# Optimization experiments

Hardware: AMD Instinct MI355X
Metric: run time of the kernel (lower is better)

Reference implementation:

```python
import jax, jax.numpy as jnp
import numpy as np

H = 256
V_IN = 32000
V_OUT = 32000
T = 2048


def setup_inputs() -> dict:
    key = jax.random.key(0)
    ks = jax.random.split(key, 16)
    s = 1.0 / np.sqrt(H)
    inp = {
        "src": jax.random.randint(ks[0], (T, 1), 0, V_IN, dtype=jnp.int64 if jax.config.jax_enable_x64 else jnp.int32),
        "trg": jax.random.randint(ks[1], (T, 1), 0, V_OUT, dtype=jnp.int64 if jax.config.jax_enable_x64 else jnp.int32),
        "enc_emb": jax.random.normal(ks[2], (V_IN, H), jnp.float32),
        "enc_W_ih": jax.random.uniform(ks[3], (3 * H, H), jnp.float32, -s, s),
        "enc_W_hh": jax.random.uniform(ks[4], (3 * H, H), jnp.float32, -s, s),
        "enc_b_ih": jax.random.uniform(ks[5], (3 * H,), jnp.float32, -s, s),
        "enc_b_hh": jax.random.uniform(ks[6], (3 * H,), jnp.float32, -s, s),
        "dec_emb": jax.random.normal(ks[7], (V_OUT, H), jnp.float32),
        "dec_W_ih": jax.random.uniform(ks[8], (3 * H, H), jnp.float32, -s, s),
        "dec_W_hh": jax.random.uniform(ks[9], (3 * H, H), jnp.float32, -s, s),
        "dec_b_ih": jax.random.uniform(ks[10], (3 * H,), jnp.float32, -s, s),
        "dec_b_hh": jax.random.uniform(ks[11], (3 * H,), jnp.float32, -s, s),
        "out_W": jax.random.uniform(ks[12], (V_OUT, H), jnp.float32, -s, s),
        "out_b": jax.random.uniform(ks[13], (V_OUT,), jnp.float32, -s, s),
    }
    return inp


def _gru_step(x, h, W_ih, W_hh, b_ih, b_hh):
    # PyTorch GRU cell math. x,h: [H]
    gi = W_ih @ x + b_ih          # [3H]
    gh = W_hh @ h + b_hh          # [3H]
    i_r, i_z, i_n = jnp.split(gi, 3)
    h_r, h_z, h_n = jnp.split(gh, 3)
    r = jax.nn.sigmoid(i_r + h_r)
    z = jax.nn.sigmoid(i_z + h_z)
    n = jnp.tanh(i_n + r * h_n)
    return (1.0 - z) * n + z * h


def reference(src, trg, enc_emb, enc_W_ih, enc_W_hh, enc_b_ih, enc_b_hh,
              dec_emb, dec_W_ih, dec_W_hh, dec_b_ih, dec_b_hh, out_W, out_b):
    src_t = src[:, 0]  # [T], batch forced to 1 by .view(1,1,-1)
    trg_t = trg[:, 0]  # [T]
    h0 = jnp.zeros((H,), enc_emb.dtype)

    def step(h, toks):
        s_tok, t_tok = toks
        # encoder step
        h = _gru_step(enc_emb[s_tok], h, enc_W_ih, enc_W_hh, enc_b_ih, enc_b_hh)
        # decoder step (relu on embedding per source)
        x_d = jax.nn.relu(dec_emb[t_tok])
        h = _gru_step(x_d, h, dec_W_ih, dec_W_hh, dec_b_ih, dec_b_hh)
        logits = out_W @ h + out_b          # [V_OUT]
        return h, jax.nn.log_softmax(logits)

    _, outs = jax.lax.scan(step, h0, (src_t, trg_t))
    return outs[:, None, :]  # [T, 1, V_OUT]
```

## Files before the change

### kernel.cpp

```cpp
#include <hip/hip_runtime.h>
#include <hip/hip_bf16.h>

#define T_STEPS 2048
#define HDIM 256
#define VOUT 32000

typedef short short8 __attribute__((ext_vector_type(8)));
typedef float f32x4 __attribute__((ext_vector_type(4)));

#if defined(__has_builtin)
#if __has_builtin(__builtin_amdgcn_sdot4)
#define HAVE_SDOT4 1
#endif
#endif

__device__ __forceinline__ int dot4i8(int a, int b, int c) {
#ifdef HAVE_SDOT4
    return __builtin_amdgcn_sdot4(a, b, c, false);
#else
#pragma unroll
    for (int k = 0; k < 4; ++k) {
        int av = (a << (24 - 8 * k)) >> 24;
        int bv = (b << (24 - 8 * k)) >> 24;
        c += av * bv;
    }
    return c;
#endif
}

__device__ __forceinline__ float fast_sigmoid(float x) {
    return 1.0f / (1.0f + __expf(-x));
}
__device__ __forceinline__ float fast_tanh(float x) {
    float ax = fabsf(x);
    float e = __expf(-2.0f * ax);
    float t = 1.0f - 2.0f * e / (1.0f + e);
    return copysignf(t, x);
}

__global__ void k_quant(const float* __restrict__ W, int* __restrict__ wq,
                        float* __restrict__ sc) {
    int row = blockIdx.x;
    int t = threadIdx.x;
    float4 w = ((const float4*)(W + (size_t)row * HDIM))[t];
    float m = fmaxf(fmaxf(fabsf(w.x), fabsf(w.y)), fmaxf(fabsf(w.z), fabsf(w.w)));
#pragma unroll
    for (int off = 32; off; off >>= 1) m = fmaxf(m, __shfl_xor(m, off));
    float inv = (m > 0.0f) ? 127.0f / m : 0.0f;
    float scale = (m > 0.0f) ? m * (1.0f / 127.0f) : 0.0f;
    int q0 = __float2int_rn(w.x * inv); q0 = max(-127, min(127, q0));
    int q1 = __float2int_rn(w.y * inv); q1 = max(-127, min(127, q1));
    int q2 = __float2int_rn(w.z * inv); q2 = max(-127, min(127, q2));
    int q3 = __float2int_rn(w.w * inv); q3 = max(-127, min(127, q3));
    int packed = (q0 & 255) | ((q1 & 255) << 8) | ((q2 & 255) << 16) | ((q3 & 255) << 24);
    wq[row * 64 + t] = packed;
    if (t == 0) sc[row] = scale;
}

__global__ __launch_bounds__(256) void k_cvt(const float* __restrict__ in,
                                             unsigned short* __restrict__ out, int n4) {
    int i = blockIdx.x * 256 + threadIdx.x;
    if (i < n4) {
        float4 v = ((const float4*)in)[i];
        unsigned int u[4] = {__float_as_uint(v.x), __float_as_uint(v.y),
                             __float_as_uint(v.z), __float_as_uint(v.w)};
        ushort4 o;
        o.x = (unsigned short)((u[0] + 0x7FFFu + ((u[0] >> 16) & 1)) >> 16);
        o.y = (unsigned short)((u[1] + 0x7FFFu + ((u[1] >> 16) & 1)) >> 16);
        o.z = (unsigned short)((u[2] + 0x7FFFu + ((u[2] >> 16) & 1)) >> 16);
        o.w = (unsigned short)((u[3] + 0x7FFFu + ((u[3] >> 16) & 1)) >> 16);
        ((ushort4*)out)[i] = o;
    }
}

__global__ __launch_bounds__(256) void k_gi(const int* __restrict__ toks,
                                            const float* __restrict__ emb,
                                            const float* __restrict__ W,
                                            const float* __restrict__ b,
                                            float* __restrict__ gi, int do_relu) {
    __shared__ float4 xs[64];
    int t = blockIdx.x;
    int tid = threadIdx.x;
    int tok = toks[t];
    if (tid < 64) {
        float4 x = ((const float4*)(emb + (size_t)tok * HDIM))[tid];
        if (do_relu) {
            x.x = fmaxf(x.x, 0.0f); x.y = fmaxf(x.y, 0.0f);
            x.z = fmaxf(x.z, 0.0f); x.w = fmaxf(x.w, 0.0f);
        }
        xs[tid] = x;
    }
    __syncthreads();
#pragma unroll
    for (int g = 0; g < 3; ++g) {
        int row = tid + g * 256;
        const float4* wr = (const float4*)(W + (size_t)row * HDIM);
        float acc = b[row];
#pragma unroll 16
        for (int k = 0; k < 64; ++k) {
            float4 w = wr[k];
            float4 x = xs[k];
            acc += w.x * x.x + w.y * x.y + w.z * x.z + w.w * x.w;
        }
        gi[(size_t)t * 768 + row] = acc;
    }
}

__global__ __launch_bounds__(768, 3) void k_gru(
    const int* __restrict__ wq_e, const float* __restrict__ sc_e,
    const float* __restrict__ bhh_e, const float* __restrict__ gi_e,
    const int* __restrict__ wq_d, const float* __restrict__ sc_d,
    const float* __restrict__ bhh_d, const float* __restrict__ gi_d,
    float* __restrict__ h_all) {
    __shared__ float Y[768];
    __shared__ float GN[256];
    __shared__ __align__(16) int HQ[64];

    const int tid = threadIdx.x;
    const int w = tid >> 6;
    const int l = tid & 63;
    const int c = l & 3;
    const int g = l >> 2;

    int we[4][16], wd[4][16];
#pragma unroll
    for (int j = 0; j < 4; ++j) {
        const int4* pe = (const int4*)(wq_e + ((w * 64 + g * 4 + j) * 64 + c * 16));
        const int4* pd = (const int4*)(wq_d + ((w * 64 + g * 4 + j) * 64 + c * 16));
#pragma unroll
        for (int i = 0; i < 4; ++i) {
            int4 a = pe[i];
            we[j][4 * i + 0] = a.x; we[j][4 * i + 1] = a.y;
            we[j][4 * i + 2] = a.z; we[j][4 * i + 3] = a.w;
            int4 bq = pd[i];
            wd[j][4 * i + 0] = bq.x; wd[j][4 * i + 1] = bq.y;
            wd[j][4 * i + 2] = bq.z; wd[j][4 * i + 3] = bq.w;
        }
    }
    const float se = sc_e[tid] * (1.0f / 127.0f);
    const float sd = sc_d[tid] * (1.0f / 127.0f);
    const float be = bhh_e[tid];
    const float bd = bhh_d[tid];
    const bool lead = (tid < 256);
    const int c0 = c & 1;
    const int c1 = c & 2;
    float h = 0.0f;
    if (tid < 64) HQ[tid] = 0;
    __syncthreads();

    const float* ge = gi_e + tid;
    const float* gd = gi_d + tid;
    float* hop = h_all + tid;
    const int4* hq4 = (const int4*)HQ;

    for (int t = 0; t < T_STEPS; ++t) {
        float gie = *ge; ge += 768;
        float gid = *gd; gd += 768;

        {
            int4 h0 = hq4[c * 4 + 0];
            int4 h1 = hq4[c * 4 + 1];
            int4 h2 = hq4[c * 4 + 2];
            int4 h3 = hq4[c * 4 + 3];
            int p[4];
#pragma unroll
            for (int j = 0; j < 4; ++j) {
                int a = 0;
                a = dot4i8(we[j][0], h0.x, a);  a = dot4i8(we[j][1], h0.y, a);
                a = dot4i8(we[j][2], h0.z, a);  a = dot4i8(we[j][3], h0.w, a);
                a = dot4i8(we[j][4], h1.x, a);  a = dot4i8(we[j][5], h1.y, a);
                a = dot4i8(we[j][6], h1.z, a);  a = dot4i8(we[j][7], h1.w, a);
                a = dot4i8(we[j][8], h2.x, a);  a = dot4i8(we[j][9], h2.y, a);
                a = dot4i8(we[j][10], h2.z, a); a = dot4i8(we[j][11], h2.w, a);
                a = dot4i8(we[j][12], h3.x, a); a = dot4i8(we[j][13], h3.y, a);
                a = dot4i8(we[j][14], h3.z, a); a = dot4i8(we[j][15], h3.w, a);
                p[j] = a;
            }
            int s0 = c0 ? p[0] : p[1];
            int s1 = c0 ? p[2] : p[3];
            int r0 = (c0 ? p[1] : p[0]) + __shfl_xor(s0, 1);
            int r1 = (c0 ? p[3] : p[2]) + __shfl_xor(s1, 1);
            int s2 = c1 ? r0 : r1;
            int fin = (c1 ? r1 : r0) + __shfl_xor(s2, 2);
            float y = se * (float)fin + be;
            if (tid < 512) Y[tid] = y + gie;
            else { Y[tid] = y; GN[tid - 512] = gie; }
        }
        __syncthreads();
        if (lead) {
            float r = fast_sigmoid(Y[tid]);
            float z = fast_sigmoid(Y[256 + tid]);
            float n = fast_tanh(GN[tid] + r * Y[512 + tid]);
            h = (1.0f - z) * n + z * h;
            ((signed char*)HQ)[tid] = (signed char)__float2int_rn(h * 127.0f);
        }
        __syncthreads();

        {
            int4 h0 = hq4[c * 4 + 0];
            int4 h1 = hq4[c * 4 + 1];
            int4 h2 = hq4[c * 4 + 2];
            int4 h3 = hq4[c * 4 + 3];
            int p[4];
#pragma unroll
            for (int j = 0; j < 4; ++j) {
                int a = 0;
                a = dot4i8(wd[j][0], h0.x, a);  a = dot4i8(wd[j][1], h0.y, a);
                a = dot4i8(wd[j][2], h0.z, a);  a = dot4i8(wd[j][3], h0.w, a);
                a = dot4i8(wd[j][4], h1.x, a);  a = dot4i8(wd[j][5], h1.y, a);
                a = dot4i8(wd[j][6], h1.z, a);  a = dot4i8(wd[j][7], h1.w, a);
                a = dot4i8(wd[j][8], h2.x, a);  a = dot4i8(wd[j][9], h2.y, a);
                a = dot4i8(wd[j][10], h2.z, a); a = dot4i8(wd[j][11], h2.w, a);
                a = dot4i8(wd[j][12], h3.x, a); a = dot4i8(wd[j][13], h3.y, a);
                a = dot4i8(wd[j][14], h3.z, a); a = dot4i8(wd[j][15], h3.w, a);
                p[j] = a;
            }
            int s0 = c0 ? p[0] : p[1];
            int s1 = c0 ? p[2] : p[3];
            int r0 = (c0 ? p[1] : p[0]) + __shfl_xor(s0, 1);
            int r1 = (c0 ? p[3] : p[2]) + __shfl_xor(s1, 1);
            int s2 = c1 ? r0 : r1;
            int fin = (c1 ? r1 : r0) + __shfl_xor(s2, 2);
            float y = sd * (float)fin + bd;
            if (tid < 512) Y[tid] = y + gid;
            else { Y[tid] = y; GN[tid - 512] = gid; }
        }
        __syncthreads();
        if (lead) {
            float r = fast_sigmoid(Y[tid]);
            float z = fast_sigmoid(Y[256 + tid]);
            float n = fast_tanh(GN[tid] + r * Y[512 + tid]);
            h = (1.0f - z) * n + z * h;
            *hop = h; hop += 256;
            ((signed char*)HQ)[tid] = (signed char)__float2int_rn(h * 127.0f);
        }
        __syncthreads();
    }
}

__global__ __launch_bounds__(256) void k_logits(const unsigned short* __restrict__ hb,
                                                const unsigned short* __restrict__ wb,
                                                const float* __restrict__ out_b,
                                                float* __restrict__ out) {
    const int vb = blockIdx.x * 64;
    const int tb = blockIdx.y * 64;
    const int w = threadIdx.x >> 6;
    const int l = threadIdx.x & 63;
    const int m = l & 15;
    const int q = l >> 4;

    const unsigned short* aptr = hb + (size_t)(tb + w * 16 + m) * HDIM + q * 8;
    const unsigned short* bptr = wb + (size_t)(vb + m) * HDIM + q * 8;

    short8 af[8];
#pragma unroll
    for (int kt = 0; kt < 8; ++kt) af[kt] = *(const short8*)(aptr + kt * 32);

    f32x4 acc[4];
#pragma unroll
    for (int nt = 0; nt < 4; ++nt)
#pragma unroll
        for (int r = 0; r < 4; ++r) acc[nt][r] = 0.0f;

#pragma unroll
    for (int nt = 0; nt < 4; ++nt) {
        const unsigned short* bp = bptr + (size_t)nt * 16 * HDIM;
#pragma unroll
        for (int kt = 0; kt < 8; ++kt) {
            short8 bf = *(const short8*)(bp + kt * 32);
            acc[nt] = __builtin_amdgcn_mfma_f32_16x16x32_bf16(af[kt], bf, acc[nt], 0, 0, 0);
        }
    }
#pragma unroll
    for (int nt = 0; nt < 4; ++nt) {
        float bias = out_b[vb + nt * 16 + m];
#pragma unroll
        for (int r = 0; r < 4; ++r) {
            out[(size_t)(tb + w * 16 + q * 4 + r) * VOUT + vb + nt * 16 + m] =
                acc[nt][r] + bias;
        }
    }
}

__global__ __launch_bounds__(256) void k_lse(const float* __restrict__ out,
                                             float* __restrict__ lse) {
    const int t = blockIdx.x;
    const int tid = threadIdx.x;
    const float* rowp = out + (size_t)t * VOUT;
    float m = -3.0e38f, l = 0.0f;
    for (int v = tid; v < VOUT; v += 256) {
        float x = rowp[v];
        float M = fmaxf(m, x);
        l = l * __expf(m - M) + __expf(x - M);
        m = M;
    }
#pragma unroll
    for (int off = 32; off; off >>= 1) {
        float m2 = __shfl_xor(m, off);
        float l2 = __shfl_xor(l, off);
        float M = fmaxf(m, m2);
        l = l * __expf(m - M) + l2 * __expf(m2 - M);
        m = M;
    }
    __shared__ float sm[4], sl[4];
    int lane = tid & 63, wv = tid >> 6;
    if (lane == 0) { sm[wv] = m; sl[wv] = l; }
    __syncthreads();
    if (tid == 0) {
        float M = fmaxf(fmaxf(sm[0], sm[1]), fmaxf(sm[2], sm[3]));
        float L = sl[0] * __expf(sm[0] - M) + sl[1] * __expf(sm[1] - M) +
                  sl[2] * __expf(sm[2] - M) + sl[3] * __expf(sm[3] - M);
        lse[t] = M + __logf(L);
    }
}

__global__ __launch_bounds__(256) void k_sub(float* __restrict__ out,
                                             const float* __restrict__ lse) {
    const int t = blockIdx.y;
    const int v4 = blockIdx.x * 256 + threadIdx.x;
    if (v4 < VOUT / 4) {
        float s = lse[t];
        float4* p = (float4*)(out + (size_t)t * VOUT) + v4;
        float4 o = *p;
        o.x -= s; o.y -= s; o.z -= s; o.w -= s;
        *p = o;
    }
}

extern "C" void kernel_launch(void* const* d_in, const int* in_sizes, int n_in,
                              void* d_out, int out_size, void* d_ws, size_t ws_size,
                              hipStream_t stream) {
    (void)in_sizes; (void)n_in; (void)out_size; (void)ws_size;
    const int*   src      = (const int*)d_in[0];
    const int*   trg      = (const int*)d_in[1];
    const float* enc_emb  = (const float*)d_in[2];
    const float* enc_W_ih = (const float*)d_in[3];
    const float* enc_W_hh = (const float*)d_in[4];
    const float* enc_b_ih = (const float*)d_in[5];
    const float* enc_b_hh = (const float*)d_in[6];
    const float* dec_emb  = (const float*)d_in[7];
    const float* dec_W_ih = (const float*)d_in[8];
    const float* dec_W_hh = (const float*)d_in[9];
    const float* dec_b_ih = (const float*)d_in[10];
    const float* dec_b_hh = (const float*)d_in[11];
    const float* out_W    = (const float*)d_in[12];
    const float* out_b    = (const float*)d_in[13];
    float* out = (float*)d_out;

    char* ws = (char*)d_ws;
    float* gi_e  = (float*)ws; ws += (size_t)T_STEPS * 768 * 4;
    float* gi_d  = (float*)ws; ws += (size_t)T_STEPS * 768 * 4;
    float* h_all = (float*)ws; ws += (size_t)T_STEPS * HDIM * 4;
    float* lse   = (float*)ws; ws += (size_t)T_STEPS * 4;
    float* sc_e  = (float*)ws; ws += 768 * 4;
    float* sc_d  = (float*)ws; ws += 768 * 4;
    int*   wq_e  = (int*)ws;   ws += 768 * 64 * 4;
    int*   wq_d  = (int*)ws;   ws += 768 * 64 * 4;
    unsigned short* h_bf = (unsigned short*)ws; ws += (size_t)T_STEPS * HDIM * 2;
    unsigned short* w_bf = (unsigned short*)ws; ws += (size_t)VOUT * HDIM * 2;

    k_quant<<<768, 64, 0, stream>>>(enc_W_hh, wq_e, sc_e);
    k_quant<<<768, 64, 0, stream>>>(dec_W_hh, wq_d, sc_d);
    k_cvt<<<(VOUT * HDIM / 4 + 255) / 256, 256, 0, stream>>>(out_W, w_bf, VOUT * HDIM / 4);
    k_gi<<<T_STEPS, 256, 0, stream>>>(src, enc_emb, enc_W_ih, enc_b_ih, gi_e, 0);
    k_gi<<<T_STEPS, 256, 0, stream>>>(trg, dec_emb, dec_W_ih, dec_b_ih, gi_d, 1);
    k_gru<<<1, 768, 0, stream>>>(wq_e, sc_e, enc_b_hh, gi_e,
                                 wq_d, sc_d, dec_b_hh, gi_d, h_all);
    k_cvt<<<(T_STEPS * HDIM / 4 + 255) / 256, 256, 0, stream>>>(h_all, h_bf, T_STEPS * HDIM / 4);
    k_logits<<<dim3(VOUT / 64, T_STEPS / 64), 256, 0, stream>>>(h_bf, w_bf, out_b, out);
    k_lse<<<T_STEPS, 256, 0, stream>>>(out, lse);
    k_sub<<<dim3(32, T_STEPS), 256, 0, stream>>>(out, lse);
}
```

Measured before the change: 4.463 ms.

## Restructure GRU recurrence to one thread per hidden unit with double-buffered state

The sequential GRU kernel moves from 768 threads (4 lanes per row, shuffle reductions, Y staging buffer) to 256 threads, each owning all three gate rows of one hidden unit. Every thread now holds 384 int8-packed weight registers and computes the gates and new state itself. This halves the barriers per step by ping-ponging between two quantized-state buffers, and it prefetches the next step's input-gate values one step ahead. The logits grid is also transposed so that consecutive blocks walk the time dimension. The cost is heavy register pressure that risks spilling, plus a longer serial dot-product chain per thread.

Measured after the change: 5.686 ms. 1.27x slower.

```diff
diff --git a/kernel.cpp b/kernel.cpp
--- a/kernel.cpp
+++ b/kernel.cpp
@@ -106,135 +106,119 @@
     }
 }
 
-__global__ __launch_bounds__(768, 3) void k_gru(
+__global__ __launch_bounds__(256, 1) void k_gru(
     const int* __restrict__ wq_e, const float* __restrict__ sc_e,
     const float* __restrict__ bhh_e, const float* __restrict__ gi_e,
     const int* __restrict__ wq_d, const float* __restrict__ sc_d,
     const float* __restrict__ bhh_d, const float* __restrict__ gi_d,
     float* __restrict__ h_all) {
-    __shared__ float Y[768];
-    __shared__ float GN[256];
-    __shared__ __align__(16) int HQ[64];
-
-    const int tid = threadIdx.x;
-    const int w = tid >> 6;
-    const int l = tid & 63;
-    const int c = l & 3;
-    const int g = l >> 2;
-
-    int we[4][16], wd[4][16];
-#pragma unroll
-    for (int j = 0; j < 4; ++j) {
-        const int4* pe = (const int4*)(wq_e + ((w * 64 + g * 4 + j) * 64 + c * 16));
-        const int4* pd = (const int4*)(wq_d + ((w * 64 + g * 4 + j) * 64 + c * 16));
-#pragma unroll
-        for (int i = 0; i < 4; ++i) {
-            int4 a = pe[i];
-            we[j][4 * i + 0] = a.x; we[j][4 * i + 1] = a.y;
-            we[j][4 * i + 2] = a.z; we[j][4 * i + 3] = a.w;
-            int4 bq = pd[i];
-            wd[j][4 * i + 0] = bq.x; wd[j][4 * i + 1] = bq.y;
-            wd[j][4 * i + 2] = bq.z; wd[j][4 * i + 3] = bq.w;
-        }
-    }
-    const float se = sc_e[tid] * (1.0f / 127.0f);
-    const float sd = sc_d[tid] * (1.0f / 127.0f);
-    const float be = bhh_e[tid];
-    const float bd = bhh_d[tid];
-    const bool lead = (tid < 256);
-    const int c0 = c & 1;
-    const int c1 = c & 2;
+    __shared__ __align__(16) int HQ0[64];
+    __shared__ __align__(16) int HQ1[64];
+
+    const int i = threadIdx.x;
+
+    int we[3][64], wd[3][64];
+#pragma unroll
+    for (int j = 0; j < 3; ++j) {
+        const int4* pe = (const int4*)(wq_e + (j * 256 + i) * 64);
+        const int4* pd = (const int4*)(wq_d + (j * 256 + i) * 64);
+#pragma unroll
+        for (int q = 0; q < 16; ++q) {
+            int4 a = pe[q];
+            we[j][4 * q + 0] = a.x; we[j][4 * q + 1] = a.y;
+            we[j][4 * q + 2] = a.z; we[j][4 * q + 3] = a.w;
+            int4 bq = pd[q];
+            wd[j][4 * q + 0] = bq.x; wd[j][4 * q + 1] = bq.y;
+            wd[j][4 * q + 2] = bq.z; wd[j][4 * q + 3] = bq.w;
+        }
+    }
+    const float ser = sc_e[i] * (1.0f / 127.0f);
+    const float sez = sc_e[256 + i] * (1.0f / 127.0f);
+    const float sen = sc_e[512 + i] * (1.0f / 127.0f);
+    const float sdr = sc_d[i] * (1.0f / 127.0f);
+    const float sdz = sc_d[256 + i] * (1.0f / 127.0f);
+    const float sdn = sc_d[512 + i] * (1.0f / 127.0f);
+    const float ber = bhh_e[i];
+    const float bez = bhh_e[256 + i];
+    const float ben = bhh_e[512 + i];
+    const float bdr = bhh_d[i];
+    const float bdz = bhh_d[256 + i];
+    const float bdn = bhh_d[512 + i];
+
     float h = 0.0f;
-    if (tid < 64) HQ[tid] = 0;
+    if (i < 64) HQ0[i] = 0;
+
+    const float* pge = gi_e + i;
+    const float* pgd = gi_d + i;
+    float ger = pge[0], gez = pge[256], gen = pge[512];
+    float gdr = pgd[0], gdz = pgd[256], gdn = pgd[512];
+    pge += 768; pgd += 768;
+    float* hop = h_all + i;
+
     __syncthreads();
 
-    const float* ge = gi_e + tid;
-    const float* gd = gi_d + tid;
-    float* hop = h_all + tid;
-    const int4* hq4 = (const int4*)HQ;
-
     for (int t = 0; t < T_STEPS; ++t) {
-        float gie = *ge; ge += 768;
-        float gid = *gd; gd += 768;
+        float n_ger = pge[0], n_gez = pge[256], n_gen = pge[512];
+        float n_gdr = pgd[0], n_gdz = pgd[256], n_gdn = pgd[512];
+        pge += 768; pgd += 768;
 
         {
-            int4 h0 = hq4[c * 4 + 0];
-            int4 h1 = hq4[c * 4 + 1];
-            int4 h2 = hq4[c * 4 + 2];
-            int4 h3 = hq4[c * 4 + 3];
-            int p[4];
-#pragma unroll
-            for (int j = 0; j < 4; ++j) {
-                int a = 0;
-                a = dot4i8(we[j][0], h0.x, a);  a = dot4i8(we[j][1], h0.y, a);
-                a = dot4i8(we[j][2], h0.z, a);  a = dot4i8(we[j][3], h0.w, a);
-                a = dot4i8(we[j][4], h1.x, a);  a = dot4i8(we[j][5], h1.y, a);
-                a = dot4i8(we[j][6], h1.z, a);  a = dot4i8(we[j][7], h1.w, a);
-                a = dot4i8(we[j][8], h2.x, a);  a = dot4i8(we[j][9], h2.y, a);
-                a = dot4i8(we[j][10], h2.z, a); a = dot4i8(we[j][11], h2.w, a);
-                a = dot4i8(we[j][12], h3.x, a); a = dot4i8(we[j][13], h3.y, a);
-                a = dot4i8(we[j][14], h3.z, a); a = dot4i8(we[j][15], h3.w, a);
-                p[j] = a;
+            int pr = 0, pz = 0, pn = 0;
+            const int4* hq = (const int4*)HQ0;
+#pragma unroll
+            for (int q = 0; q < 16; ++q) {
+                int4 a = hq[q];
+                pr = dot4i8(we[0][4 * q + 0], a.x, pr);
+                pr = dot4i8(we[0][4 * q + 1], a.y, pr);
+                pr = dot4i8(we[0][4 * q + 2], a.z, pr);
+                pr = dot4i8(we[0][4 * q + 3], a.w, pr);
+                pz = dot4i8(we[1][4 * q + 0], a.x, pz);
+                pz = dot4i8(we[1][4 * q + 1], a.y, pz);
+                pz = dot4i8(we[1][4 * q + 2], a.z, pz);
+                pz = dot4i8(we[1][4 * q + 3], a.w, pz);
+                pn = dot4i8(we[2][4 * q + 0], a.x, pn);
+                pn = dot4i8(we[2][4 * q + 1], a.y, pn);
+                pn = dot4i8(we[2][4 * q + 2], a.z, pn);
+                pn = dot4i8(we[2][4 * q + 3], a.w, pn);
             }
-            int s0 = c0 ? p[0] : p[1];
-            int s1 = c0 ? p[2] : p[3];
-            int r0 = (c0 ? p[1] : p[0]) + __shfl_xor(s0, 1);
-            int r1 = (c0 ? p[3] : p[2]) + __shfl_xor(s1, 1);
-            int s2 = c1 ? r0 : r1;
-            int fin = (c1 ? r1 : r0) + __shfl_xor(s2, 2);
-            float y = se * (float)fin + be;
-            if (tid < 512) Y[tid] = y + gie;
-            else { Y[tid] = y; GN[tid - 512] = gie; }
+            float r = fast_sigmoid(ser * (float)pr + ber + ger);
+            float z = fast_sigmoid(sez * (float)pz + bez + gez);
+            float n = fast_tanh(gen + r * (sen * (float)pn + ben));
+            h = (1.0f - z) * n + z * h;
+            ((signed char*)HQ1)[i] = (signed char)__float2int_rn(h * 127.0f);
         }
         __syncthreads();
-        if (lead) {
-            float r = fast_sigmoid(Y[tid]);
-            float z = fast_sigmoid(Y[256 + tid]);
-            float n = fast_tanh(GN[tid] + r * Y[512 + tid]);
-            h = (1.0f - z) * n + z * h;
-            ((signed char*)HQ)[tid] = (signed char)__float2int_rn(h * 127.0f);
-        }
-        __syncthreads();
 
         {
-            int4 h0 = hq4[c * 4 + 0];
-            int4 h1 = hq4[c * 4 + 1];
-            int4 h2 = hq4[c * 4 + 2];
-            int4 h3 = hq4[c * 4 + 3];
-            int p[4];
-#pragma unroll
-            for (int j = 0; j < 4; ++j) {
-                int a = 0;
-                a = dot4i8(wd[j][0], h0.x, a);  a = dot4i8(wd[j][1], h0.y, a);
-                a = dot4i8(wd[j][2], h0.z, a);  a = dot4i8(wd[j][3], h0.w, a);
-                a = dot4i8(wd[j][4], h1.x, a);  a = dot4i8(wd[j][5], h1.y, a);
-                a = dot4i8(wd[j][6], h1.z, a);  a = dot4i8(wd[j][7], h1.w, a);
-                a = dot4i8(wd[j][8], h2.x, a);  a = dot4i8(wd[j][9], h2.y, a);
-                a = dot4i8(wd[j][10], h2.z, a); a = dot4i8(wd[j][11], h2.w, a);
-                a = dot4i8(wd[j][12], h3.x, a); a = dot4i8(wd[j][13], h3.y, a);
-                a = dot4i8(wd[j][14], h3.z, a); a = dot4i8(wd[j][15], h3.w, a);
-                p[j] = a;
+            int pr = 0, pz = 0, pn = 0;
+            const int4* hq = (const int4*)HQ1;
+#pragma unroll
+            for (int q = 0; q < 16; ++q) {
+                int4 a = hq[q];
+                pr = dot4i8(wd[0][4 * q + 0], a.x, pr);
+                pr = dot4i8(wd[0][4 * q + 1], a.y, pr);
+                pr = dot4i8(wd[0][4 * q + 2], a.z, pr);
+                pr = dot4i8(wd[0][4 * q + 3], a.w, pr);
+                pz = dot4i8(wd[1][4 * q + 0], a.x, pz);
+                pz = dot4i8(wd[1][4 * q + 1], a.y, pz);
+                pz = dot4i8(wd[1][4 * q + 2], a.z, pz);
+                pz = dot4i8(wd[1][4 * q + 3], a.w, pz);
+                pn = dot4i8(wd[2][4 * q + 0], a.x, pn);
+                pn = dot4i8(wd[2][4 * q + 1], a.y, pn);
+                pn = dot4i8(wd[2][4 * q + 2], a.z, pn);
+                pn = dot4i8(wd[2][4 * q + 3], a.w, pn);
             }
-            int s0 = c0 ? p[0] : p[1];
-            int s1 = c0 ? p[2] : p[3];
-            int r0 = (c0 ? p[1] : p[0]) + __shfl_xor(s0, 1);
-            int r1 = (c0 ? p[3] : p[2]) + __shfl_xor(s1, 1);
-            int s2 = c1 ? r0 : r1;
-            int fin = (c1 ? r1 : r0) + __shfl_xor(s2, 2);
-            float y = sd * (float)fin + bd;
-            if (tid < 512) Y[tid] = y + gid;
-            else { Y[tid] = y; GN[tid - 512] = gid; }
-        }
-        __syncthreads();
-        if (lead) {
-            float r = fast_sigmoid(Y[tid]);
-            float z = fast_sigmoid(Y[256 + tid]);
-            float n = fast_tanh(GN[tid] + r * Y[512 + tid]);
+            float r = fast_sigmoid(sdr * (float)pr + bdr + gdr);
+            float z = fast_sigmoid(sdz * (float)pz + bdz + gdz);
+            float n = fast_tanh(gdn + r * (sdn * (float)pn + bdn));
             h = (1.0f - z) * n + z * h;
             *hop = h; hop += 256;
-            ((signed char*)HQ)[tid] = (signed char)__float2int_rn(h * 127.0f);
+            ((signed char*)HQ0)[i] = (signed char)__float2int_rn(h * 127.0f);
         }
         __syncthreads();
+
+        ger = n_ger; gez = n_gez; gen = n_gen;
+        gdr = n_gdr; gdz = n_gdz; gdn = n_gdn;
     }
 }
 
@@ -242,8 +226,8 @@
                                                 const unsigned short* __restrict__ wb,
                                                 const float* __restrict__ out_b,
                                                 float* __restrict__ out) {
-    const int vb = blockIdx.x * 64;
-    const int tb = blockIdx.y * 64;
+    const int tb = blockIdx.x * 64;
+    const int vb = blockIdx.y * 64;
     const int w = threadIdx.x >> 6;
     const int l = threadIdx.x & 63;
     const int m = l & 15;
@@ -348,8 +332,8 @@
     float* out = (float*)d_out;
 
     char* ws = (char*)d_ws;
-    float* gi_e  = (float*)ws; ws += (size_t)T_STEPS * 768 * 4;
-    float* gi_d  = (float*)ws; ws += (size_t)T_STEPS * 768 * 4;
+    float* gi_e  = (float*)ws; ws += (size_t)(T_STEPS + 1) * 768 * 4;
+    float* gi_d  = (float*)ws; ws += (size_t)(T_STEPS + 1) * 768 * 4;
     float* h_all = (float*)ws; ws += (size_t)T_STEPS * HDIM * 4;
     float* lse   = (float*)ws; ws += (size_t)T_STEPS * 4;
     float* sc_e  = (float*)ws; ws += 768 * 4;
@@ -364,10 +348,10 @@
     k_cvt<<<(VOUT * HDIM / 4 + 255) / 256, 256, 0, stream>>>(out_W, w_bf, VOUT * HDIM / 4);
     k_gi<<<T_STEPS, 256, 0, stream>>>(src, enc_emb, enc_W_ih, enc_b_ih, gi_e, 0);
     k_gi<<<T_STEPS, 256, 0, stream>>>(trg, dec_emb, dec_W_ih, dec_b_ih, gi_d, 1);
-    k_gru<<<1, 768, 0, stream>>>(wq_e, sc_e, enc_b_hh, gi_e,
+    k_gru<<<1, 256, 0, stream>>>(wq_e, sc_e, enc_b_hh, gi_e,
                                  wq_d, sc_d, dec_b_hh, gi_d, h_all);
     k_cvt<<<(T_STEPS * HDIM / 4 + 255) / 256, 256, 0, stream>>>(h_all, h_bf, T_STEPS * HDIM / 4);
-    k_logits<<<dim3(VOUT / 64, T_STEPS / 64), 256, 0, stream>>>(h_bf, w_bf, out_b, out);
+    k_logits<<<dim3(T_STEPS / 64, VOUT / 64), 256, 0, stream>>>(h_bf, w_bf, out_b, out);
     k_lse<<<T_STEPS, 256, 0, stream>>>(out, lse);
     k_sub<<<dim3(32, T_STEPS), 256, 0, stream>>>(out, lse);
 }
```
